# Performance work log

Measured on AMD Instinct MI355X. Metric: run time of the kernel, lower is better.

## Reference

```python
import jax, jax.numpy as jnp
import numpy as np
import math

B, T, D = 8, 2048, 1024
H, DH = 16, 64
DI = H * DH
EPS = 1e-6
LN_EPS = 1e-5


def setup_inputs() -> dict:
    key = jax.random.key(0)
    ks = jax.random.split(key, 8)
    def xavier(k, shape):
        fan_in, fan_out = shape[0], shape[1]
        bound = math.sqrt(6.0 / (fan_in + fan_out))
        return jax.random.uniform(k, shape, jnp.float32, -bound, bound)
    x = jax.random.normal(ks[0], (B, T, D), jnp.float32)
    Wq = xavier(ks[1], (D, DI))
    Wk = xavier(ks[2], (D, DI))
    Wv = xavier(ks[3], (D, DI))
    Wa = jax.random.normal(ks[4], (D, DI), jnp.float32) * 0.02
    ba = jnp.full((DI,), 3.0, jnp.float32)
    Wb = jax.random.normal(ks[5], (D, H), jnp.float32) * 0.02
    bb = jnp.zeros((H,), jnp.float32)
    raw_gamma_m = jnp.full((H,), math.log(0.99 / 0.01), jnp.float32)
    Wo = xavier(ks[6], (DI, D))
    ln_g = jnp.ones((D,), jnp.float32)
    ln_b = jnp.zeros((D,), jnp.float32)
    return {"x": x, "ln_g": ln_g, "ln_b": ln_b, "Wq": Wq, "Wk": Wk, "Wv": Wv,
            "Wa": Wa, "ba": ba, "Wb": Wb, "bb": bb,
            "raw_gamma_m": raw_gamma_m, "Wo": Wo}


def _layernorm(x, g, b):
    mu = jnp.mean(x, axis=-1, keepdims=True)
    var = jnp.mean(jnp.square(x - mu), axis=-1, keepdims=True)
    return (x - mu) * jax.lax.rsqrt(var + LN_EPS) * g + b


def _sokda_scan(q, k, v, alpha, beta, gamma_m):
    # q,k,v,alpha: (B,H,T,d); beta: (B,H,T); gamma_m: (H,)
    d = q.shape[-1]
    S0 = jnp.zeros((B, H, d, d), q.dtype)
    M0 = EPS * jnp.broadcast_to(jnp.eye(d, dtype=q.dtype), (B, H, d, d))
    gm = gamma_m[None, :, None, None]  # (1,H,1,1)

    def step(carry, xs):
        S, M = carry
        k_t, v_t, q_t, a_t, b_t = xs  # (B,H,d)x4, (B,H)
        kn = k_t / jnp.maximum(jnp.linalg.norm(k_t, axis=-1, keepdims=True), 1e-12)
        M = gm * M + kn[..., :, None] * kn[..., None, :]
        Mk = jnp.einsum('bhij,bhj->bhi', M, kn)
        k_tilde = Mk / jnp.maximum(jnp.linalg.norm(Mk, axis=-1, keepdims=True), EPS)
        S = a_t[..., None] * S  # diag(alpha) scaling of rows
        kproj = jnp.einsum('bhd,bhde->bhe', kn, S)  # k^T S
        bexp = b_t[..., None, None]
        S = S - bexp * k_tilde[..., :, None] * kproj[..., None, :]
        S = S + bexp * kn[..., :, None] * v_t[..., None, :]
        o = jnp.einsum('bhji,bhj->bhi', S, q_t)  # S^T q
        return (S, M), o

    # move time to leading axis for scan
    xs = (jnp.moveaxis(k, 2, 0), jnp.moveaxis(v, 2, 0), jnp.moveaxis(q, 2, 0),
          jnp.moveaxis(alpha, 2, 0), jnp.moveaxis(beta, 2, 0))
    _, outs = jax.lax.scan(step, (S0, M0), xs)  # outs: (T,B,H,d)
    return jnp.moveaxis(outs, 0, 2)  # (B,H,T,d)


def reference(x, ln_g, ln_b, Wq, Wk, Wv, Wa, ba, Wb, bb, raw_gamma_m, Wo):
    residual = x
    xn = _layernorm(x, ln_g, ln_b)
    def heads(y):
        return jnp.transpose(y.reshape(B, T, H, DH), (0, 2, 1, 3))  # (B,H,T,d)
    q = heads(xn @ Wq)
    k = heads(xn @ Wk)
    v = heads(xn @ Wv)
    alpha = jax.nn.sigmoid(heads(xn @ Wa + ba))
    beta = jnp.transpose(jax.nn.sigmoid(xn @ Wb + bb), (0, 2, 1))  # (B,H,T)
    gamma_m = jax.nn.sigmoid(raw_gamma_m)
    out = _sokda_scan(q, k, v, alpha, beta, gamma_m)  # (B,H,T,d)
    out = jnp.transpose(out, (0, 2, 1, 3)).reshape(B, T, DI)
    out = out @ Wo  # dropout is identity in eval mode
    return out + residual
```

## Files before the change

kernel.cpp:

```cpp
#include <hip/hip_runtime.h>

typedef unsigned short u16;
typedef unsigned int   u32;
typedef _Float16       f16;
typedef __attribute__((ext_vector_type(4))) _Float16 v4h;
typedef __attribute__((ext_vector_type(8))) _Float16 v8h;
typedef __attribute__((ext_vector_type(4))) float    v4f;

#define TT 2048
#define BB 8

static __device__ __forceinline__ float sigmoidf_(float x){
    return 1.0f / (1.0f + __expf(-x));
}
static __device__ __forceinline__ float allreduce64(float v){
    #pragma unroll
    for (int off = 32; off > 0; off >>= 1) v += __shfl_xor(v, off, 64);
    return v;
}

static __device__ __forceinline__ float wave_sum64(float x){
    int t;
    t = __builtin_amdgcn_update_dpp(0, __float_as_int(x), 0x111, 0xf, 0xf, true); x += __int_as_float(t);
    t = __builtin_amdgcn_update_dpp(0, __float_as_int(x), 0x112, 0xf, 0xf, true); x += __int_as_float(t);
    t = __builtin_amdgcn_update_dpp(0, __float_as_int(x), 0x114, 0xf, 0xf, true); x += __int_as_float(t);
    t = __builtin_amdgcn_update_dpp(0, __float_as_int(x), 0x118, 0xf, 0xf, true); x += __int_as_float(t);
    t = __builtin_amdgcn_update_dpp(0, __float_as_int(x), 0x142, 0xf, 0xf, true); x += __int_as_float(t);
    t = __builtin_amdgcn_update_dpp(0, __float_as_int(x), 0x143, 0xf, 0xf, true); x += __int_as_float(t);
    return __int_as_float(__builtin_amdgcn_readlane(__float_as_int(x), 63));
}

__global__ __launch_bounds__(256) void sentinel_fill(float* __restrict__ out, int n){
    int i = blockIdx.x * 256 + threadIdx.x;
    if (i < n) out[i] = 12345.0f;
}

__global__ __launch_bounds__(256) void ln_kernel(
    const float* __restrict__ x, const float* __restrict__ g,
    const float* __restrict__ bta, f16* __restrict__ xn)
{
    const int row = blockIdx.x;
    const int tid = threadIdx.x;
    const float4 v = ((const float4*)(x + (size_t)row * 1024))[tid];
    float s  = v.x + v.y + v.z + v.w;
    float s2 = v.x*v.x + v.y*v.y + v.z*v.z + v.w*v.w;
    #pragma unroll
    for (int off = 32; off > 0; off >>= 1){
        s  += __shfl_xor(s,  off, 64);
        s2 += __shfl_xor(s2, off, 64);
    }
    __shared__ float rs[4], rq[4];
    const int wv = tid >> 6, lane = tid & 63;
    if (lane == 0){ rs[wv] = s; rq[wv] = s2; }
    __syncthreads();
    s  = rs[0] + rs[1] + rs[2] + rs[3];
    s2 = rq[0] + rq[1] + rq[2] + rq[3];
    const float mu   = s * (1.0f / 1024.0f);
    const float var  = s2 * (1.0f / 1024.0f) - mu * mu;
    const float rstd = rsqrtf(var + 1e-5f);
    const float4 gv = ((const float4*)g)[tid];
    const float4 bv = ((const float4*)bta)[tid];
    v4h o;
    o.x = (f16)((v.x - mu) * rstd * gv.x + bv.x);
    o.y = (f16)((v.y - mu) * rstd * gv.y + bv.y);
    o.z = (f16)((v.z - mu) * rstd * gv.z + bv.z);
    o.w = (f16)((v.w - mu) * rstd * gv.w + bv.w);
    ((v4h*)(xn + (size_t)row * 1024))[tid] = o;
}

__global__ __launch_bounds__(256) void transpose5(
    const float* __restrict__ Wq, const float* __restrict__ Wk,
    const float* __restrict__ Wv, const float* __restrict__ Wa,
    const float* __restrict__ Wo, f16* __restrict__ wcat, f16* __restrict__ wot)
{
    __shared__ float tile[32][33];
    const int z = blockIdx.z;
    const float* src = (z==0)?Wq:(z==1)?Wk:(z==2)?Wv:(z==3)?Wa:Wo;
    f16* dst = (z < 4) ? (wcat + (size_t)z * 1024 * 1024) : wot;
    const int bx = blockIdx.x * 32, by = blockIdx.y * 32;
    const int tx = threadIdx.x, ty = threadIdx.y;
    #pragma unroll
    for (int i = 0; i < 4; ++i)
        tile[ty + i*8][tx] = src[(size_t)(by + ty + i*8) * 1024 + bx + tx];
    __syncthreads();
    #pragma unroll
    for (int i = 0; i < 4; ++i)
        dst[(size_t)(bx + ty + i*8) * 1024 + by + tx] = (f16)tile[tx][ty + i*8];
}

template<int MODE>
__global__ __launch_bounds__(256) void gemm_bt(
    const f16* __restrict__ A, const f16* __restrict__ Bt,
    int M, int N, int K,
    const float* __restrict__ ba, const float* __restrict__ resid,
    float* __restrict__ Cf,
    f16* __restrict__ Qb, f16* __restrict__ Kb,
    f16* __restrict__ Vb, f16* __restrict__ Ab)
{
    __shared__ f16 As[128 * 72];
    __shared__ f16 Bs[128 * 72];
    const int tid = threadIdx.x;
    const int bm = blockIdx.x, bn = blockIdx.y;
    const int wv = tid >> 6, lane = tid & 63;
    const int l15 = lane & 15, quad = lane >> 4;
    const int mb = (wv >> 1) * 64, nb = (wv & 1) * 64;
    v4f acc[4][4];
    const v4f vzero = {0.0f, 0.0f, 0.0f, 0.0f};
    #pragma unroll
    for (int i = 0; i < 4; ++i)
        #pragma unroll
        for (int j = 0; j < 4; ++j) acc[i][j] = vzero;

    const f16* Ag = A  + (size_t)bm * 128 * K;
    const f16* Bg = Bt + (size_t)bn * 128 * K;

    for (int k0 = 0; k0 < K; k0 += 64){
        __syncthreads();
        #pragma unroll
        for (int it = 0; it < 4; ++it){
            const int ch = tid + it * 256;
            const int r = ch >> 3, c = ch & 7;
            const uint4 da = *(const uint4*)(Ag + (size_t)r * K + k0 + c * 8);
            *(uint4*)(&As[r * 72 + c * 8]) = da;
            const uint4 db = *(const uint4*)(Bg + (size_t)r * K + k0 + c * 8);
            *(uint4*)(&Bs[r * 72 + c * 8]) = db;
        }
        __syncthreads();
        #pragma unroll
        for (int kk = 0; kk < 2; ++kk){
            v8h af[4], bfr[4];
            #pragma unroll
            for (int i = 0; i < 4; ++i){
                af[i]  = *(const v8h*)(&As[(mb + i*16 + l15) * 72 + kk*32 + quad*8]);
                bfr[i] = *(const v8h*)(&Bs[(nb + i*16 + l15) * 72 + kk*32 + quad*8]);
            }
            #pragma unroll
            for (int i = 0; i < 4; ++i)
                #pragma unroll
                for (int j = 0; j < 4; ++j)
                    acc[i][j] = __builtin_amdgcn_mfma_f32_16x16x32_f16(af[i], bfr[j], acc[i][j], 0, 0, 0);
        }
    }
    const int seg = (bn * 128) >> 10;
    f16* dst = (seg == 0) ? Qb : (seg == 1) ? Kb : (seg == 2) ? Vb : Ab;
    #pragma unroll
    for (int i = 0; i < 4; ++i){
        #pragma unroll
        for (int j = 0; j < 4; ++j){
            const int col = bn * 128 + nb + j * 16 + l15;
            const int c   = col & 1023;
            #pragma unroll
            for (int r = 0; r < 4; ++r){
                const int row = bm * 128 + mb + i * 16 + quad * 4 + r;
                float val = acc[i][j][r];
                if (MODE == 0){
                    if (seg == 3) val = sigmoidf_(val + ba[c]);
                    dst[(size_t)row * 1024 + c] = (f16)val;
                } else {
                    Cf[(size_t)row * N + col] = val + resid[(size_t)row * N + col];
                }
            }
        }
    }
}

__global__ __launch_bounds__(256) void beta_kernel(
    const f16* __restrict__ xn, const float* __restrict__ Wb,
    const float* __restrict__ bb, float* __restrict__ betaw)
{
    const int row = blockIdx.x;
    const int b = row >> 11, t = row & 2047;
    const int wv = threadIdx.x >> 6, lane = threadIdx.x & 63;
    const f16* xr = xn + (size_t)row * 1024;
    #pragma unroll
    for (int hh = 0; hh < 4; ++hh){
        const int h = wv * 4 + hh;
        float acc = 0.0f;
        #pragma unroll 4
        for (int k = lane; k < 1024; k += 64)
            acc += (float)xr[k] * Wb[k * 16 + h];
        acc = allreduce64(acc);
        if (lane == 0)
            betaw[((size_t)(b * 16 + h)) * 2048 + t] = sigmoidf_(acc + bb[h]);
    }
}

#define SC 16
__global__ __launch_bounds__(512, 2) void scan_kernel(
    const f16* __restrict__ Qb, const f16* __restrict__ Kb,
    const f16* __restrict__ Vb, const f16* __restrict__ Ab,
    const float* __restrict__ beta, const float* __restrict__ rgm,
    f16* __restrict__ O)
{
    const int chain = blockIdx.x;
    const int b = chain >> 4, h = chain & 15;
    const int tid = threadIdx.x;
    const int wid = __builtin_amdgcn_readfirstlane(tid) >> 6;
    const int l = tid & 63;
    const float gm = sigmoidf_(rgm[h]);
    const int l15 = l & 15, q4 = l >> 4;

    __shared__ f16 tQ[1024], tK[1024], tV[1024], tA[1024];
    __shared__ float betaT[SC], rnkT[SC], gmps[20];
    __shared__ float GcT[64*18], IGcT[64*18], ktlTT[64*18];
    __shared__ f16 KnAh[16*72], KnAl[16*72];
    __shared__ f16 KnBcat[16*136];
    __shared__ f16 KnTcat[64*40], KnTEcat[64*40];
    __shared__ f16 Dcat[16*40];
    __shared__ f16 M0h[64*72], M0l[64*72];
    __shared__ f16 PhT[16*72], PlT[16*72], QhT[16*72], QlT[16*72];
    __shared__ f16 Wcat[16*136], Ucat[16*136];
    __shared__ f16 WTcat[64*40], UTcat[64*40];
    __shared__ f16 HTcat[64*40];
    __shared__ f16 VT[64*24];
    __shared__ f16 ZTcat[64*136];
    __shared__ f16 Cmcat[3*16*40];
    __shared__ float Hs[16*68], Ob[16*68];
    __shared__ float C2s[16*17];

    const size_t cbase = ((size_t)(b * TT)) * 1024 + h * 64;
    const int tens = tid >> 7, rem = tid & 127;
    const int str = rem >> 3, j4 = rem & 7;
    const f16* sg = (tens == 0) ? Qb : (tens == 1) ? Kb : (tens == 2) ? Vb : Ab;
    f16* sl = (tens == 0) ? tQ : (tens == 1) ? tK : (tens == 2) ? tV : tA;

    {
        const uint4 d0 = *(const uint4*)(sg + cbase + (size_t)str * 1024 + j4 * 8);
        *(uint4*)(sl + str * 64 + j4 * 8) = d0;
        if (tid < SC) betaT[tid] = beta[(size_t)chain * TT + tid];
        for (int i = tid; i < 64*136; i += 512) ZTcat[i] = (f16)0.0f;
        for (int i = tid; i < 64*72; i += 512){ M0h[i] = (f16)0.0f; M0l[i] = (f16)0.0f; }
        if (tid == 0){
            float g = 1.0f;
            #pragma unroll
            for (int k = 0; k <= 16; ++k){ gmps[k] = g; g *= gm; }
        }
    }
    __syncthreads();
    if (tid < 64) M0h[tid * 73] = (f16)1e-6f;

    #pragma unroll 1
    for (int t0 = 0; t0 < TT; t0 += SC){
        __syncthreads();

        #pragma unroll
        for (int rr = 0; rr < 2; ++rr){
            const int t = (wid << 1) + rr;
            const float kv = (float)tK[t * 64 + l];
            const float nk = wave_sum64(kv * kv);
            if (l == 0) rnkT[t] = __builtin_amdgcn_rcpf(fmaxf(sqrtf(nk), 1e-12f));
        }
        if (wid == 7){
            float g = 1.0f;
            #pragma unroll
            for (int t = 0; t < SC; ++t){
                g *= (float)tA[t * 64 + l];
                GcT[l * 18 + t]  = g;
                IGcT[l * 18 + t] = __builtin_amdgcn_rcpf(g);
            }
        }
        __syncthreads();

        #pragma unroll
        for (int half = 0; half < 2; ++half){
            const int idx = tid + half * 512;
            {
                const int t = idx >> 6, d = idx & 63;
                const float kn = (float)tK[t * 64 + d] * rnkT[t];
                const f16 kh = (f16)kn; const f16 kl = (f16)(kn - (float)kh);
                KnAh[t * 72 + d] = kh;  KnAl[t * 72 + d] = kl;
                const int cc = ((d >> 4) << 5) + (d & 15);
                KnBcat[t * 136 + cc] = kh;  KnBcat[t * 136 + cc + 16] = kl;
            }
            {
                const int d2 = idx >> 4, t2 = idx & 15;
                const float kn2 = (float)tK[t2 * 64 + d2] * rnkT[t2];
                const f16 kh2 = (f16)kn2;
                KnTcat[d2 * 40 + t2]      = kh2;
                KnTcat[d2 * 40 + 16 + t2] = (f16)(kn2 - (float)kh2);
                const float ke = kn2 * gmps[15 - t2];
                const f16 keh = (f16)ke;
                KnTEcat[d2 * 40 + t2]      = keh;
                KnTEcat[d2 * 40 + 16 + t2] = (f16)(ke - (float)keh);
            }
            {
                const int e = idx & 63, i2 = idx >> 6;
                VT[e * 24 + i2] = tV[i2 * 64 + e];
            }
        }
        __syncthreads();

        if (wid == 0){
            const int ar = l15 * 72 + (q4 & 1) * 8;
            const int br = l15 * 136 + q4 * 8;
            v4f g4 = {0.f, 0.f, 0.f, 0.f};
            #pragma unroll
            for (int c = 0; c < 4; ++c)
                g4 = __builtin_amdgcn_mfma_f32_16x16x32_f16(
                        *(const v8h*)(KnAh + ar + c * 16),
                        *(const v8h*)(KnBcat + br + c * 32), g4, 0, 0, 0);
            #pragma unroll
            for (int c = 0; c < 4; ++c)
                g4 = __builtin_amdgcn_mfma_f32_16x16x32_f16(
                        *(const v8h*)(KnAl + ar + c * 16),
                        *(const v8h*)(KnBcat + br + c * 32), g4, 0, 0, 0);
            #pragma unroll
            for (int j = 0; j < 4; ++j){
                const int t = q4 * 4 + j, i = l15;
                const float dv = (i <= t) ? g4[j] * gmps[t - i] : 0.0f;
                const f16 dh = (f16)dv;
                Dcat[t * 40 + i]      = dh;
                Dcat[t * 40 + 16 + i] = (f16)(dv - (float)dh);
            }
        } else if (wid <= 4){
            const int rt = wid - 1;
            const int ar = (rt * 16 + l15) * 72 + (q4 & 1) * 8;
            const int br = l15 * 136 + q4 * 8;
            v4f acc = {0.f, 0.f, 0.f, 0.f};
            #pragma unroll
            for (int c = 0; c < 4; ++c)
                acc = __builtin_amdgcn_mfma_f32_16x16x32_f16(
                        *(const v8h*)(M0h + ar + c * 16),
                        *(const v8h*)(KnBcat + br + c * 32), acc, 0, 0, 0);
            #pragma unroll
            for (int c = 0; c < 4; ++c)
                acc = __builtin_amdgcn_mfma_f32_16x16x32_f16(
                        *(const v8h*)(M0l + ar + c * 16),
                        *(const v8h*)(KnBcat + br + c * 32), acc, 0, 0, 0);
            #pragma unroll
            for (int j = 0; j < 4; ++j)
                Hs[(rt * 16 + q4 * 4 + j) * 17 + l15] = acc[j];
        }
        __syncthreads();

        if (wid < 4){
            const int et = wid;
            const int arD = l15 * 40 + (q4 & 1) * 8;
            const int brD = (et * 16 + l15) * 40 + q4 * 8;
            v4f acc = {0.f, 0.f, 0.f, 0.f};
            acc = __builtin_amdgcn_mfma_f32_16x16x32_f16(
                    *(const v8h*)(Dcat + arD), *(const v8h*)(KnTcat + brD), acc, 0, 0, 0);
            acc = __builtin_amdgcn_mfma_f32_16x16x32_f16(
                    *(const v8h*)(Dcat + arD + 16), *(const v8h*)(KnTcat + brD), acc, 0, 0, 0);
            #pragma unroll
            for (int j = 0; j < 4; ++j){
                const int t = q4 * 4 + j, d = et * 16 + l15;
                Ob[t * 68 + d] = acc[j] + gmps[t + 1] * Hs[d * 17 + t];
            }
        } else {
            #pragma unroll
            for (int k = 0; k < 4; ++k){
                const int idx = (tid - 256) + k * 256;
                const int t = idx >> 6, d = idx & 63;
                const float g  = GcT[d * 18 + t];
                const float ig = IGcT[d * 18 + t];
                const float kn = (float)tK[t * 64 + d] * rnkT[t];
                const float bt = betaT[t];
                const float pv = kn * g;
                const float qv = (float)tQ[t * 64 + d] * g;
                const float wv = bt * kn * ig;
                const f16 ph = (f16)pv, qh = (f16)qv, wh = (f16)wv;
                PhT[t * 72 + d] = ph;  PlT[t * 72 + d] = (f16)(pv - (float)ph);
                QhT[t * 72 + d] = qh;  QlT[t * 72 + d] = (f16)(qv - (float)qh);
                const int cc = ((d >> 4) << 5) + (d & 15);
                Wcat[t * 136 + cc] = wh;  Wcat[t * 136 + cc + 16] = (f16)(wv - (float)wh);
            }
        }
        __syncthreads();

        #pragma unroll
        for (int rr = 0; rr < 2; ++rr){
            const int t = (wid << 1) + rr;
            const float x = Ob[t * 68 + l];
            const float nm = wave_sum64(x * x);
            ktlTT[l * 18 + t] = x * __builtin_amdgcn_rcpf(fmaxf(sqrtf(nm), 1e-6f));
        }
        __syncthreads();

        if (wid < 4){
            #pragma unroll
            for (int k = 0; k < 4; ++k){
                const int idx = tid + k * 256;
                const int t = idx >> 6, d = idx & 63;
                const float uv = betaT[t] * ktlTT[d * 18 + t] * IGcT[d * 18 + t];
                const f16 uh = (f16)uv;
                const int cc = ((d >> 4) << 5) + (d & 15);
                Ucat[t * 136 + cc] = uh;  Ucat[t * 136 + cc + 16] = (f16)(uv - (float)uh);
            }
        } else {
            #pragma unroll
            for (int k = 0; k < 4; ++k){
                const int idx = (tid - 256) + k * 256;
                const int d = idx >> 4, t = idx & 15;
                const float ig = IGcT[d * 18 + t];
                const float bt = betaT[t];
                const float kn = (float)KnTcat[d * 40 + t] + (float)KnTcat[d * 40 + 16 + t];
                const float wv = bt * kn * ig;
                const f16 wh = (f16)wv;
                WTcat[d * 40 + t]      = wh;
                WTcat[d * 40 + 16 + t] = (f16)(wv - (float)wh);
                const float nu = -(bt * ktlTT[d * 18 + t] * ig);
                const f16 nuh = (f16)nu;
                UTcat[d * 40 + t]      = nuh;
                UTcat[d * 40 + 16 + t] = (f16)(nu - (float)nuh);
            }
        }
        __syncthreads();

        {
            const int et = wid & 3;
            const f16* Amh = (wid < 4) ? PhT : QhT;
            const f16* Aml = (wid < 4) ? PlT : QlT;
            const int ar = l15 * 72 + (q4 & 1) * 8;
            const int br = (et * 16 + l15) * 136 + q4 * 8;
            v4f acc = {0.f, 0.f, 0.f, 0.f};
            #pragma unroll
            for (int c = 0; c < 4; ++c){
                const v8h ah = *(const v8h*)(Amh + ar + c * 16);
                const v8h al = *(const v8h*)(Aml + ar + c * 16);
                const v8h bz = *(const v8h*)(ZTcat + br + c * 32);
                acc = __builtin_amdgcn_mfma_f32_16x16x32_f16(ah, bz, acc, 0, 0, 0);
                acc = __builtin_amdgcn_mfma_f32_16x16x32_f16(al, bz, acc, 0, 0, 0);
            }
            float* Rdst = (wid < 4) ? Hs : Ob;
            #pragma unroll
            for (int j = 0; j < 4; ++j)
                Rdst[(q4 * 4 + j) * 68 + et * 16 + l15] = acc[j];

            if (wid < 4){
                const f16* A2h = (wid < 2) ? PhT : QhT;
                const f16* A2l = (wid < 2) ? PlT : QlT;
                const f16* Bp  = (wid & 1) ? Ucat : Wcat;
                const int br2 = l15 * 136 + q4 * 8;
                v4f pacc = {0.f, 0.f, 0.f, 0.f};
                #pragma unroll
                for (int c = 0; c < 4; ++c){
                    const v8h a2h = *(const v8h*)(A2h + ar + c * 16);
                    const v8h a2l = *(const v8h*)(A2l + ar + c * 16);
                    const v8h bw  = *(const v8h*)(Bp + br2 + c * 32);
                    pacc = __builtin_amdgcn_mfma_f32_16x16x32_f16(a2h, bw, pacc, 0, 0, 0);
                    pacc = __builtin_amdgcn_mfma_f32_16x16x32_f16(a2l, bw, pacc, 0, 0, 0);
                }
                if (wid == 1){
                    #pragma unroll
                    for (int j = 0; j < 4; ++j)
                        C2s[(q4 * 4 + j) * 17 + l15] = pacc[j];
                } else {
                    const int mm = (wid == 0) ? 0 : (wid == 2) ? 1 : 2;
                    #pragma unroll
                    for (int j = 0; j < 4; ++j){
                        const int t = q4 * 4 + j, i = l15;
                        float v = ((mm == 0) ? (i < t) : (i <= t)) ? pacc[j] : 0.0f;
                        if (mm == 2) v = -v;
                        const f16 vh = (f16)v;
                        Cmcat[mm * 640 + t * 40 + i] = vh;
                        Cmcat[mm * 640 + t * 40 + 16 + i] = (f16)(v - (float)vh);
                    }
                }
            }
        }
        __syncthreads();

        {
            const int et = wid & 3;
            const int mm = (wid < 4) ? 0 : 1;
            float* Rd = (wid < 4) ? Hs : Ob;
            const v8h ac = *(const v8h*)(Cmcat + mm * 640 + l15 * 40 + q4 * 8);
            const v8h bv = *(const v8h*)(VT + (et * 16 + l15) * 24 + (q4 & 1) * 8);
            v4f acc;
            #pragma unroll
            for (int j = 0; j < 4; ++j) acc[j] = Rd[(q4 * 4 + j) * 68 + et * 16 + l15];
            acc = __builtin_amdgcn_mfma_f32_16x16x32_f16(ac, bv, acc, 0, 0, 0);
            #pragma unroll
            for (int j = 0; j < 4; ++j) Rd[(q4 * 4 + j) * 68 + et * 16 + l15] = acc[j];
        }
        __syncthreads();

        if (wid == 0){
            float rhs[SC];
            #pragma unroll
            for (int t = 0; t < SC; ++t) rhs[t] = Hs[t * 68 + l];
            float hreg[SC];
            #pragma unroll
            for (int t = 0; t < SC; ++t){
                float x = rhs[t];
                #pragma unroll
                for (int i = 0; i < SC; ++i)
                    if (i < t) x = fmaf(-C2s[t * 17 + i], hreg[i], x);
                hreg[t] = x;
                const f16 hh = (f16)x;
                HTcat[l * 40 + t] = hh;
                HTcat[l * 40 + 16 + t] = (f16)(x - (float)hh);
            }
        } else {
            if (t0 + SC < TT){
                const int base = tid - 64;
                #pragma unroll
                for (int rep = 0; rep < 2; ++rep){
                    const int ch = base + rep * 448;
                    if (ch < 512){
                        const int tens2 = ch >> 7, rem2 = ch & 127;
                        const int str2 = rem2 >> 3, jj = rem2 & 7;
                        const f16* sgp = (tens2 == 0) ? Qb : (tens2 == 1) ? Kb : (tens2 == 2) ? Vb : Ab;
                        f16* slp = (tens2 == 0) ? tQ : (tens2 == 1) ? tK : (tens2 == 2) ? tV : tA;
                        const uint4 dd0 = *(const uint4*)(sgp + cbase + (size_t)(t0 + SC + str2) * 1024 + jj * 8);
                        *(uint4*)(slp + str2 * 64 + jj * 8) = dd0;
                    }
                }
                if (base < SC) betaT[base] = beta[(size_t)chain * TT + t0 + SC + base];
            }
            const float gm16 = gmps[16];
            #pragma unroll
            for (int r = 0; r < 3; ++r){
                const int tile = (wid - 1) + 7 * r;
                if (tile < 16){
                    const int rt = tile >> 2, ct = tile & 3;
                    const int ar = (rt * 16 + l15) * 40 + (q4 & 1) * 8;
                    const int br = (ct * 16 + l15) * 40 + q4 * 8;
                    v4f acc;
                    #pragma unroll
                    for (int j = 0; j < 4; ++j){
                        const int row = rt * 16 + q4 * 4 + j, col = ct * 16 + l15;
                        acc[j] = gm16 * ((float)M0h[row * 72 + col] + (float)M0l[row * 72 + col]);
                    }
                    acc = __builtin_amdgcn_mfma_f32_16x16x32_f16(
                            *(const v8h*)(KnTcat + ar), *(const v8h*)(KnTEcat + br), acc, 0, 0, 0);
                    acc = __builtin_amdgcn_mfma_f32_16x16x32_f16(
                            *(const v8h*)(KnTcat + ar + 16), *(const v8h*)(KnTEcat + br), acc, 0, 0, 0);
                    #pragma unroll
                    for (int j = 0; j < 4; ++j){
                        const int row = rt * 16 + q4 * 4 + j, col = ct * 16 + l15;
                        const float v = acc[j];
                        const f16 vh = (f16)v;
                        M0h[row * 72 + col] = vh;
                        M0l[row * 72 + col] = (f16)(v - (float)vh);
                    }
                }
            }
        }
        __syncthreads();

        {
            const int et = wid & 3;
            const int arow = et * 16 + l15;
            const v8h aV  = *(const v8h*)(VT + arow * 24 + (q4 & 1) * 8);
            const v8h aHh = *(const v8h*)(HTcat + arow * 40 + (q4 & 1) * 8);
            const v8h aHl = *(const v8h*)(HTcat + arow * 40 + 16 + (q4 & 1) * 8);

            if (wid < 4){
                const v8h aC = *(const v8h*)(Cmcat + 2 * 640 + l15 * 40 + q4 * 8);
                v4f acc2;
                #pragma unroll
                for (int j = 0; j < 4; ++j) acc2[j] = Ob[(q4 * 4 + j) * 68 + et * 16 + l15];
                acc2 = __builtin_amdgcn_mfma_f32_16x16x32_f16(aC, aHh, acc2, 0, 0, 0);
                acc2 = __builtin_amdgcn_mfma_f32_16x16x32_f16(aC, aHl, acc2, 0, 0, 0);
                #pragma unroll
                for (int j = 0; j < 4; ++j){
                    const int t = q4 * 4 + j;
                    O[cbase + (size_t)(t0 + t) * 1024 + et * 16 + l15] = (f16)acc2[j];
                }
            }

            #pragma unroll
            for (int tt2 = 0; tt2 < 2; ++tt2){
                const int dt = (wid >> 2) * 2 + tt2;
                const v8h bW = *(const v8h*)(WTcat + (dt * 16 + l15) * 40 + q4 * 8);
                const v8h bU = *(const v8h*)(UTcat + (dt * 16 + l15) * 40 + q4 * 8);
                v4f acc;
                #pragma unroll
                for (int j = 0; j < 4; ++j){
                    const int er = et * 16 + q4 * 4 + j;
                    acc[j] = (float)ZTcat[er * 136 + dt * 32 + l15]
                           + (float)ZTcat[er * 136 + dt * 32 + 16 + l15];
                }
                acc = __builtin_amdgcn_mfma_f32_16x16x32_f16(aV,  bW, acc, 0, 0, 0);
                acc = __builtin_amdgcn_mfma_f32_16x16x32_f16(aHh, bU, acc, 0, 0, 0);
                acc = __builtin_amdgcn_mfma_f32_16x16x32_f16(aHl, bU, acc, 0, 0, 0);
                const float gl = GcT[(dt * 16 + l15) * 18 + 15];
                #pragma unroll
                for (int j = 0; j < 4; ++j){
                    const float z = acc[j] * gl;
                    const int er = et * 16 + q4 * 4 + j;
                    const f16 zh = (f16)z;
                    ZTcat[er * 136 + dt * 32 + l15] = zh;
                    ZTcat[er * 136 + dt * 32 + 16 + l15] = (f16)(z - (float)zh);
                }
            }
        }
    }
}

#define OFF_XN    ((size_t)0)
#define OFF_WCAT  ((size_t)33554432)
#define OFF_WOT   ((size_t)41943040)
#define OFF_BETA  ((size_t)44040192)
#define OFF_V     ((size_t)45088768)
#define OFF_A     ((size_t)78643200)
#define WS_NEED   ((size_t)112197632)

extern "C" void kernel_launch(void* const* d_in, const int* in_sizes, int n_in,
                              void* d_out, int out_size, void* d_ws, size_t ws_size,
                              hipStream_t stream)
{
    const float* x   = (const float*)d_in[0];
    const float* lng = (const float*)d_in[1];
    const float* lnb = (const float*)d_in[2];
    const float* Wq  = (const float*)d_in[3];
    const float* Wk  = (const float*)d_in[4];
    const float* Wv  = (const float*)d_in[5];
    const float* Wa  = (const float*)d_in[6];
    const float* ba  = (const float*)d_in[7];
    const float* Wb  = (const float*)d_in[8];
    const float* bb  = (const float*)d_in[9];
    const float* rgm = (const float*)d_in[10];
    const float* Wo  = (const float*)d_in[11];
    float* out = (float*)d_out;

    if (ws_size < WS_NEED){
        sentinel_fill<<<(out_size + 255) / 256, 256, 0, stream>>>(out, out_size);
        return;
    }

    char* ws = (char*)d_ws;
    f16*   xn   = (f16*)(ws + OFF_XN);
    f16*   wcat = (f16*)(ws + OFF_WCAT);
    f16*   wot  = (f16*)(ws + OFF_WOT);
    float* betw = (float*)(ws + OFF_BETA);
    f16*   Vbuf = (f16*)(ws + OFF_V);
    f16*   Abuf = (f16*)(ws + OFF_A);
    f16*   Qbuf = (f16*)d_out;
    f16*   Kbuf = Qbuf + (size_t)16384 * 1024;
    f16*   Obuf = xn;

    ln_kernel<<<16384, 256, 0, stream>>>(x, lng, lnb, xn);
    transpose5<<<dim3(32, 32, 5), dim3(32, 8), 0, stream>>>(Wq, Wk, Wv, Wa, Wo, wcat, wot);
    gemm_bt<0><<<dim3(128, 32), 256, 0, stream>>>(xn, wcat, 16384, 4096, 1024,
                                                  ba, nullptr, nullptr, Qbuf, Kbuf, Vbuf, Abuf);
    beta_kernel<<<16384, 256, 0, stream>>>(xn, Wb, bb, betw);
    scan_kernel<<<128, 512, 0, stream>>>(Qbuf, Kbuf, Vbuf, Abuf, betw, rgm, Obuf);
    gemm_bt<1><<<dim3(128, 8), 256, 0, stream>>>(Obuf, wot, 16384, 1024, 1024,
                                                 nullptr, x, out, nullptr, nullptr, nullptr, nullptr);
}
```

Measured before the change: 1.711 ms.

## Use direct global-to-LDS loads and swizzled block order in projection GEMM

The GEMM tile loads now use global_load_lds to write straight into shared memory, skipping the register round trip. The LDS row stride drops from 72 to 64 to suit that load pattern. Workgroup IDs are remapped with a swizzle so neighbouring blocks share A/B tiles in cache. Without the padding, the MFMA fragment reads from LDS may hit bank conflicts, and the operand loads in the scan kernel are inlined with no real effect.

```diff
diff --git a/kernel.cpp b/kernel.cpp
--- a/kernel.cpp
+++ b/kernel.cpp
@@ -97,10 +97,14 @@
     f16* __restrict__ Qb, f16* __restrict__ Kb,
     f16* __restrict__ Vb, f16* __restrict__ Ab)
 {
-    __shared__ f16 As[128 * 72];
-    __shared__ f16 Bs[128 * 72];
+    __shared__ f16 As[128 * 64];
+    __shared__ f16 Bs[128 * 64];
     const int tid = threadIdx.x;
-    const int bm = blockIdx.x, bn = blockIdx.y;
+    const int gx  = gridDim.x;
+    const int nwg = gx * gridDim.y;
+    const int fid = blockIdx.y * gx + blockIdx.x;
+    const int swz = (fid & 7) * (nwg >> 3) + (fid >> 3);
+    const int bm = swz % gx, bn = swz / gx;
     const int wv = tid >> 6, lane = tid & 63;
     const int l15 = lane & 15, quad = lane >> 4;
     const int mb = (wv >> 1) * 64, nb = (wv & 1) * 64;
@@ -113,17 +117,19 @@
 
     const f16* Ag = A  + (size_t)bm * 128 * K;
     const f16* Bg = Bt + (size_t)bn * 128 * K;
+    const int sr = lane >> 3, sc = lane & 7;
 
     for (int k0 = 0; k0 < K; k0 += 64){
         __syncthreads();
         #pragma unroll
-        for (int it = 0; it < 4; ++it){
-            const int ch = tid + it * 256;
-            const int r = ch >> 3, c = ch & 7;
-            const uint4 da = *(const uint4*)(Ag + (size_t)r * K + k0 + c * 8);
-            *(uint4*)(&As[r * 72 + c * 8]) = da;
-            const uint4 db = *(const uint4*)(Bg + (size_t)r * K + k0 + c * 8);
-            *(uint4*)(&Bs[r * 72 + c * 8]) = db;
+        for (int i = 0; i < 4; ++i){
+            const int r0 = wv * 32 + i * 8;
+            __builtin_amdgcn_global_load_lds(
+                (const __attribute__((address_space(1))) void*)(Ag + (size_t)(r0 + sr) * K + k0 + sc * 8),
+                (__attribute__((address_space(3))) void*)(As + r0 * 64), 16, 0, 0);
+            __builtin_amdgcn_global_load_lds(
+                (const __attribute__((address_space(1))) void*)(Bg + (size_t)(r0 + sr) * K + k0 + sc * 8),
+                (__attribute__((address_space(3))) void*)(Bs + r0 * 64), 16, 0, 0);
         }
         __syncthreads();
         #pragma unroll
@@ -131,8 +137,8 @@
             v8h af[4], bfr[4];
             #pragma unroll
             for (int i = 0; i < 4; ++i){
-                af[i]  = *(const v8h*)(&As[(mb + i*16 + l15) * 72 + kk*32 + quad*8]);
-                bfr[i] = *(const v8h*)(&Bs[(nb + i*16 + l15) * 72 + kk*32 + quad*8]);
+                af[i]  = *(const v8h*)(&As[(mb + i*16 + l15) * 64 + kk*32 + quad*8]);
+                bfr[i] = *(const v8h*)(&Bs[(nb + i*16 + l15) * 64 + kk*32 + quad*8]);
             }
             #pragma unroll
             for (int i = 0; i < 4; ++i)
@@ -416,11 +422,9 @@
             v4f acc = {0.f, 0.f, 0.f, 0.f};
             #pragma unroll
             for (int c = 0; c < 4; ++c){
-                const v8h ah = *(const v8h*)(Amh + ar + c * 16);
-                const v8h al = *(const v8h*)(Aml + ar + c * 16);
                 const v8h bz = *(const v8h*)(ZTcat + br + c * 32);
-                acc = __builtin_amdgcn_mfma_f32_16x16x32_f16(ah, bz, acc, 0, 0, 0);
-                acc = __builtin_amdgcn_mfma_f32_16x16x32_f16(al, bz, acc, 0, 0, 0);
+                acc = __builtin_amdgcn_mfma_f32_16x16x32_f16(*(const v8h*)(Amh + ar + c*16), bz, acc, 0, 0, 0);
+                acc = __builtin_amdgcn_mfma_f32_16x16x32_f16(*(const v8h*)(Aml + ar + c*16), bz, acc, 0, 0, 0);
             }
             float* Rdst = (wid < 4) ? Hs : Ob;
             #pragma unroll
@@ -435,11 +439,9 @@
                 v4f pacc = {0.f, 0.f, 0.f, 0.f};
                 #pragma unroll
                 for (int c = 0; c < 4; ++c){
-                    const v8h a2h = *(const v8h*)(A2h + ar + c * 16);
-                    const v8h a2l = *(const v8h*)(A2l + ar + c * 16);
                     const v8h bw  = *(const v8h*)(Bp + br2 + c * 32);
-                    pacc = __builtin_amdgcn_mfma_f32_16x16x32_f16(a2h, bw, pacc, 0, 0, 0);
-                    pacc = __builtin_amdgcn_mfma_f32_16x16x32_f16(a2l, bw, pacc, 0, 0, 0);
+                    pacc = __builtin_amdgcn_mfma_f32_16x16x32_f16(*(const v8h*)(A2h + ar + c*16), bw, pacc, 0, 0, 0);
+                    pacc = __builtin_amdgcn_mfma_f32_16x16x32_f16(*(const v8h*)(A2l + ar + c*16), bw, pacc, 0, 0, 0);
                 }
                 if (wid == 1){
                     #pragma unroll
```

New measurement: 1.790 ms. 4.6% more time.
